# Kernel optimization log

Hardware: AMD Instinct MI355X
Metric: run time of the kernel (lower is better)

The kernel has to match this reference:

```python
import jax, jax.numpy as jnp
import numpy as np

B, L, D = 2, 2048, 1024
H = 16
DEPTH = D // H  # 64
MAX_REL = 2048


def _make_relative_embedding():
    length = max(MAX_REL, DEPTH)
    r = np.arange(length)
    mat = np.clip(r[None, :] - r[:, None], -MAX_REL, MAX_REL) + MAX_REL
    return jnp.asarray(mat[:MAX_REL, :DEPTH], dtype=jnp.float32)


def setup_inputs() -> dict:
    key = jax.random.key(0)
    ks = jax.random.split(key, 8)
    query = jax.random.normal(ks[0], (B, L, D), dtype=jnp.float32)
    k_in = jax.random.normal(ks[1], (B, L, D), dtype=jnp.float32)
    v_in = jax.random.normal(ks[2], (B, L, D), dtype=jnp.float32)
    mask = jnp.tril(jnp.ones((L, L), dtype=bool))  # causal mask (memory_len, memory_len)
    Wq = jax.random.normal(ks[3], (D, D), dtype=jnp.float32) * 0.02
    bq = jnp.zeros((D,), dtype=jnp.float32)
    Wo = jax.random.normal(ks[4], (D, D), dtype=jnp.float32) * 0.02
    bo = jnp.zeros((D,), dtype=jnp.float32)
    rel_emb = _make_relative_embedding()  # [MAX_REL, DEPTH]
    return {"query": query, "key": k_in, "value": v_in, "mask": mask,
            "Wq": Wq, "bq": bq, "Wo": Wo, "bo": bo, "rel_emb": rel_emb}


def _split_heads(x):
    b, l, _ = x.shape
    return x.reshape(b, l, H, DEPTH).transpose(0, 2, 1, 3)  # [b,h,l,depth]


def _skew(rel_logits, length_k):
    # rel_logits: [b,h,Lq,Lq] (square by construction)
    b, h, lq, _ = rel_logits.shape
    x = jnp.pad(rel_logits, ((0, 0), (0, 0), (0, 0), (1, 0)))  # pad left on last dim
    x = x.reshape(b, h, lq + 1, lq)[:, :, 1:, :]
    if length_k > lq:
        x = jnp.pad(x, ((0, 0), (0, 0), (0, 0), (0, length_k - lq)))
    elif length_k < lq:
        x = x[:, :, :, :length_k]
    return x


def reference(query, key, value, mask, Wq, bq, Wo, bo, rel_emb):
    # NOTE: the source module (faithfully) uses query_projection for Q, K and V.
    q = _split_heads(query @ Wq.T + bq)   # [b,h,Lq,d]
    k = _split_heads(key @ Wq.T + bq)     # [b,h,Lk,d]
    v = _split_heads(value @ Wq.T + bq)   # [b,h,Lk,d]
    length_q, length_k = q.shape[2], k.shape[2]

    logits = jnp.einsum('bhqd,bhkd->bhqk', q, k)
    # relative embedding slice: last `length_q` rows (length_q <= MAX_REL)
    start = max(0, MAX_REL - length_q)
    key_rel = rel_emb[start:, :]                            # [Lq, d]
    rel_logits = jnp.einsum('bhld,md->bhlm', q, key_rel)    # [b,h,Lq,Lq]
    rel_logits = _skew(rel_logits, length_k)
    logits = (logits + rel_logits) / jnp.sqrt(jnp.float32(DEPTH))
    logits = jnp.where(mask, logits, jnp.float32(-1e9))
    weights = jax.nn.softmax(logits, axis=-1)               # dropout = identity (eval)
    out = jnp.einsum('bhqk,bhkd->bhqd', weights, v)
    out = out.transpose(0, 2, 1, 3).reshape(out.shape[0], -1, D)
    return out @ Wo.T + bo, weights
```

## Files before the change

### kernel.cpp

```cpp
#include <hip/hip_runtime.h>
#include <cstdint>

#define BB 2
#define LL 2048
#define DD 1024
#define HH 16
#define DH 64
#define BH 32
#define MPROJ 12288
#define MOUT 4096

typedef __attribute__((ext_vector_type(8))) short bhalf8;
typedef __attribute__((ext_vector_type(4))) float f32x4;

__device__ __forceinline__ unsigned short f2bf(float f) {
  union { float f; unsigned u; } c; c.f = f;
  unsigned u = c.u;
  u = (u + 0x7fffu + ((u >> 16) & 1u)) >> 16;
  return (unsigned short)u;
}

constexpr size_t OFF_XBF    = 0;
constexpr size_t OFF_WQBF   = OFF_XBF    + (size_t)MPROJ*DD*2;
constexpr size_t OFF_WOBF   = OFF_WQBF   + (size_t)DD*DD*2;
constexpr size_t OFF_QBF    = OFF_WOBF   + (size_t)DD*DD*2;
constexpr size_t OFF_KBF    = OFF_QBF    + (size_t)BH*LL*DH*2;
constexpr size_t OFF_VTBF   = OFF_KBF    + (size_t)BH*LL*DH*2;
constexpr size_t OFF_ATTNBF = OFF_VTBF   + (size_t)BH*LL*DH*2;
constexpr size_t OFF_WAS    = OFF_ATTNBF + (size_t)MOUT*DD*2;
constexpr size_t OFF_BAS    = OFF_WAS    + (size_t)2*HH*DD*4;
constexpr size_t OFF_AARR   = OFF_BAS    + 256;
constexpr size_t OFF_SARR   = OFF_AARR   + (size_t)BH*LL*4;
constexpr size_t OFF_MARR   = OFF_SARR   + (size_t)BH*LL*4;
constexpr size_t OFF_ZARR   = OFF_MARR   + (size_t)BH*LL*4;
constexpr size_t WS_NEED    = OFF_ZARR   + (size_t)BH*LL*4;

__global__ __launch_bounds__(256) void cast_f32_bf16(
    const float* __restrict__ src, unsigned short* __restrict__ dst, int n4) {
  int i = blockIdx.x * 256 + threadIdx.x;
  if (i < n4) {
    float4 v = ((const float4*)src)[i];
    ushort4 o;
    o.x = f2bf(v.x); o.y = f2bf(v.y); o.z = f2bf(v.z); o.w = f2bf(v.w);
    ((ushort4*)dst)[i] = o;
  }
}

__global__ __launch_bounds__(256) void prep_rel(
    const float* __restrict__ Wq, const float* __restrict__ bq,
    const float* __restrict__ rel, float* __restrict__ wAS, float* __restrict__ bAS) {
  int idx = blockIdx.x * 256 + threadIdx.x;
  if (idx >= 2 * HH * DD) return;
  int kind = idx >> 14;
  int h = (idx >> 10) & 15;
  int c = idx & 1023;
  double s = 0.0;
  for (int d = 0; d < DH; ++d) {
    double coef = kind ? 1.0 : (double)rel[d];
    s += coef * (double)Wq[(size_t)(h * DH + d) * DD + c];
  }
  wAS[idx] = (float)s;
  if (c == 0) {
    double b = 0.0;
    for (int d = 0; d < DH; ++d) {
      double coef = kind ? 1.0 : (double)rel[d];
      b += coef * (double)bq[h * DH + d];
    }
    bAS[kind * HH + h] = (float)b;
  }
}

__global__ __launch_bounds__(256) void rel_AS(
    const float* __restrict__ query, const float* __restrict__ wAS,
    const float* __restrict__ bAS, float* __restrict__ A_arr, float* __restrict__ S_arr) {
  int r = blockIdx.x * 8 + (threadIdx.x >> 5);
  int j = threadIdx.x & 31;
  const float* qrow = query + (size_t)r * DD;
  const float* w = wAS + (size_t)j * DD;
  double s = 0.0;
  for (int k = 0; k < DD; k += 4) {
    float4 qv = *(const float4*)(qrow + k);
    float4 wv = *(const float4*)(w + k);
    s += (double)qv.x * wv.x + (double)qv.y * wv.y +
         (double)qv.z * wv.z + (double)qv.w * wv.w;
  }
  s += (double)bAS[j];
  int b = r >> 11, l = r & 2047;
  int h = j & 15;
  size_t idx = (size_t)(b * HH + h) * LL + l;
  if (j >> 4) S_arr[idx] = (float)s; else A_arr[idx] = (float)s;
}

template <int EPI>
__global__ __launch_bounds__(256) void gemm_bt(
    const unsigned short* __restrict__ A, const unsigned short* __restrict__ Bm,
    const float* __restrict__ bias,
    unsigned short* __restrict__ q_bf, unsigned short* __restrict__ k_bf,
    unsigned short* __restrict__ vt_bf, float* __restrict__ outp) {
  __shared__ unsigned short lA[2][128 * 32];
  __shared__ unsigned short lB[2][128 * 32];
  const int bi = blockIdx.x, bj = blockIdx.y;
  const int t = threadIdx.x;
  const int w = t >> 6, lane = t & 63;
  const int lr = lane & 15, kg = lane >> 4;
  const int wr = w >> 1, wc = w & 1;

  const int srow = t >> 1, scol = (t & 1) * 16;
  const unsigned short* gA = A + (size_t)(bi * 128 + srow) * DD + scol;
  const unsigned short* gB = Bm + (size_t)(bj * 128 + srow) * DD + scol;
  const int soff = srow * 32 + scol;

  const f32x4 Z4 = {0.f, 0.f, 0.f, 0.f};
  f32x4 acc[4][4];
#pragma unroll
  for (int m = 0; m < 4; ++m)
#pragma unroll
    for (int n = 0; n < 4; ++n) acc[m][n] = Z4;

  {
    uint4 ra0 = *(const uint4*)(gA);
    uint4 ra1 = *(const uint4*)(gA + 8);
    uint4 rb0 = *(const uint4*)(gB);
    uint4 rb1 = *(const uint4*)(gB + 8);
    *(uint4*)&lA[0][soff] = ra0; *(uint4*)&lA[0][soff + 8] = ra1;
    *(uint4*)&lB[0][soff] = rb0; *(uint4*)&lB[0][soff + 8] = rb1;
  }
  __syncthreads();

  int cur = 0;
  for (int kt = 0; kt < 32; ++kt) {
    uint4 ra0, ra1, rb0, rb1;
    const bool more = (kt + 1 < 32);
    if (more) {
      const int k0 = (kt + 1) * 32;
      ra0 = *(const uint4*)(gA + k0);
      ra1 = *(const uint4*)(gA + k0 + 8);
      rb0 = *(const uint4*)(gB + k0);
      rb1 = *(const uint4*)(gB + k0 + 8);
    }
    bhalf8 af[4], bf[4];
#pragma unroll
    for (int m = 0; m < 4; ++m)
      af[m] = *(const bhalf8*)&lA[cur][(wr * 64 + m * 16 + lr) * 32 + kg * 8];
#pragma unroll
    for (int n = 0; n < 4; ++n)
      bf[n] = *(const bhalf8*)&lB[cur][(wc * 64 + n * 16 + lr) * 32 + kg * 8];
#pragma unroll
    for (int m = 0; m < 4; ++m)
#pragma unroll
      for (int n = 0; n < 4; ++n)
        acc[m][n] = __builtin_amdgcn_mfma_f32_16x16x32_bf16(af[m], bf[n], acc[m][n], 0, 0, 0);
    if (more) {
      *(uint4*)&lA[cur ^ 1][soff] = ra0; *(uint4*)&lA[cur ^ 1][soff + 8] = ra1;
      *(uint4*)&lB[cur ^ 1][soff] = rb0; *(uint4*)&lB[cur ^ 1][soff + 8] = rb1;
    }
    __syncthreads();
    cur ^= 1;
  }

#pragma unroll
  for (int n = 0; n < 4; ++n) {
    const int gcol = bj * 128 + wc * 64 + n * 16 + lr;
    const float bv = bias[gcol];
#pragma unroll
    for (int m = 0; m < 4; ++m) {
#pragma unroll
      for (int r = 0; r < 4; ++r) {
        const int grow = bi * 128 + wr * 64 + m * 16 + kg * 4 + r;
        float v = acc[m][n][r] + bv;
        if (EPI == 0) {
          const int src = grow >> 12;
          const int rl = grow & 4095;
          const int b = rl >> 11, l2 = rl & 2047;
          const int h = gcol >> 6, d = gcol & 63;
          const int bh = b * HH + h;
          unsigned short bfv = f2bf(v);
          if (src == 0)      q_bf[((size_t)bh * LL + l2) * DH + d] = bfv;
          else if (src == 1) k_bf[((size_t)bh * LL + l2) * DH + d] = bfv;
          else               vt_bf[((size_t)bh * DH + d) * LL + l2] = bfv;
        } else {
          outp[(size_t)grow * DD + gcol] = v;
        }
      }
    }
  }
}


__global__ __launch_bounds__(256) void attn_a(
    const unsigned short* __restrict__ q_bf, const unsigned short* __restrict__ k_bf,
    const float* __restrict__ A_arr, const float* __restrict__ S_arr,
    float* __restrict__ M_arr, float* __restrict__ Zinv_arr) {
  __shared__ unsigned short lK[2][64 * 64];
  const int bid = blockIdx.x;
  const int bh = bid & 31, qt = 31 - (bid >> 5);
  const int t = threadIdx.x, w = t >> 6, lane = t & 63;
  const int lr = lane & 15, kg = lane >> 4;
  const int qrow0 = qt * 64 + w * 16;

  const unsigned short* qbase = q_bf + ((size_t)bh * LL + qrow0 + lr) * DH + kg * 8;
  bhalf8 aq0 = *(const bhalf8*)qbase;
  bhalf8 aq1 = *(const bhalf8*)(qbase + 32);

  float Av[4], Sv[4], Mr[4], ps[4];
  int myrow[4];
#pragma unroll
  for (int r = 0; r < 4; ++r) {
    myrow[r] = qrow0 + kg * 4 + r;
    Av[r] = A_arr[(size_t)bh * LL + myrow[r]];
    Sv[r] = S_arr[(size_t)bh * LL + myrow[r]];
    Mr[r] = -INFINITY; ps[r] = 0.f;
  }

  const int srow = t >> 2, scol = (t & 3) * 16;
  const int se0 = srow * 64 + ((((t & 3) * 2 + 0) ^ (srow & 7)) * 8);
  const int se1 = srow * 64 + ((((t & 3) * 2 + 1) ^ (srow & 7)) * 8);
  const unsigned short* kbase = k_bf + (size_t)bh * LL * DH;
  const f32x4 Z4 = {0.f, 0.f, 0.f, 0.f};

  {
    const unsigned short* src = kbase + (size_t)srow * DH + scol;
    uint4 v0 = *(const uint4*)src;
    uint4 v1 = *(const uint4*)(src + 8);
    *(uint4*)&lK[0][se0] = v0;
    *(uint4*)&lK[0][se1] = v1;
  }

  int cur = 0;
  for (int kt = 0; kt <= qt; ++kt) {
    __syncthreads();
    uint4 n0, n1;
    const bool more = (kt < qt);
    if (more) {
      const unsigned short* src = kbase + (size_t)((kt + 1) * 64 + srow) * DH + scol;
      n0 = *(const uint4*)src;
      n1 = *(const uint4*)(src + 8);
    }
    f32x4 acc[4];
#pragma unroll
    for (int n = 0; n < 4; ++n) {
      acc[n] = Z4;
      const int rowb = n * 16 + lr;
      bhalf8 b0 = *(const bhalf8*)&lK[cur][rowb * 64 + ((kg ^ (rowb & 7)) * 8)];
      bhalf8 b1 = *(const bhalf8*)&lK[cur][rowb * 64 + (((4 + kg) ^ (rowb & 7)) * 8)];
      acc[n] = __builtin_amdgcn_mfma_f32_16x16x32_bf16(aq0, b0, acc[n], 0, 0, 0);
      acc[n] = __builtin_amdgcn_mfma_f32_16x16x32_bf16(aq1, b1, acc[n], 0, 0, 0);
    }
    float lg[4][4];
#pragma unroll
    for (int n = 0; n < 4; ++n) {
      const int gcol = kt * 64 + n * 16 + lr;
#pragma unroll
      for (int r = 0; r < 4; ++r) {
        float rel = Av[r] - (float)(2047 - myrow[r] + gcol) * Sv[r];
        float l = (acc[n][r] + rel) * 0.125f;
        lg[n][r] = (gcol <= myrow[r]) ? l : -1e30f;
      }
    }
#pragma unroll
    for (int r = 0; r < 4; ++r) {
      float tmax = fmaxf(fmaxf(lg[0][r], lg[1][r]), fmaxf(lg[2][r], lg[3][r]));
      tmax = fmaxf(tmax, __shfl_xor(tmax, 1));
      tmax = fmaxf(tmax, __shfl_xor(tmax, 2));
      tmax = fmaxf(tmax, __shfl_xor(tmax, 4));
      tmax = fmaxf(tmax, __shfl_xor(tmax, 8));
      float Mn = fmaxf(Mr[r], tmax);
      float s = ps[r] * __expf(Mr[r] - Mn);
      s += __expf(lg[0][r] - Mn) + __expf(lg[1][r] - Mn) +
           __expf(lg[2][r] - Mn) + __expf(lg[3][r] - Mn);
      ps[r] = s; Mr[r] = Mn;
    }
    if (more) {
      *(uint4*)&lK[cur ^ 1][se0] = n0;
      *(uint4*)&lK[cur ^ 1][se1] = n1;
    }
    cur ^= 1;
  }
#pragma unroll
  for (int r = 0; r < 4; ++r) {
    float s = ps[r];
    s += __shfl_xor(s, 1); s += __shfl_xor(s, 2);
    s += __shfl_xor(s, 4); s += __shfl_xor(s, 8);
    if (lr == 0) {
      M_arr[(size_t)bh * LL + myrow[r]] = Mr[r];
      Zinv_arr[(size_t)bh * LL + myrow[r]] = 1.0f / s;
    }
  }
}

__global__ __launch_bounds__(256) void attn_b(
    const unsigned short* __restrict__ q_bf, const unsigned short* __restrict__ k_bf,
    const unsigned short* __restrict__ vt_bf,
    const float* __restrict__ A_arr, const float* __restrict__ S_arr,
    const float* __restrict__ M_arr, const float* __restrict__ Zinv_arr,
    float* __restrict__ w_out, unsigned short* __restrict__ attn_bf) {
  __shared__ unsigned short lK[2][64 * 64];
  __shared__ unsigned short lW[64][72];
  const int bid = blockIdx.x;
  const int bh = bid & 31, qt = 31 - (bid >> 5);
  const int t = threadIdx.x, w = t >> 6, lane = t & 63;
  const int lr = lane & 15, kg = lane >> 4;
  const int qrow0 = qt * 64 + w * 16;

  const unsigned short* qbase = q_bf + ((size_t)bh * LL + qrow0 + lr) * DH + kg * 8;
  bhalf8 aq0 = *(const bhalf8*)qbase;
  bhalf8 aq1 = *(const bhalf8*)(qbase + 32);

  float Av[4], Sv[4], Mv[4], Zv[4];
  int myrow[4];
#pragma unroll
  for (int r = 0; r < 4; ++r) {
    myrow[r] = qrow0 + kg * 4 + r;
    Av[r] = A_arr[(size_t)bh * LL + myrow[r]];
    Sv[r] = S_arr[(size_t)bh * LL + myrow[r]];
    Mv[r] = M_arr[(size_t)bh * LL + myrow[r]];
    Zv[r] = Zinv_arr[(size_t)bh * LL + myrow[r]];
  }

  const f32x4 Z4 = {0.f, 0.f, 0.f, 0.f};
  f32x4 oacc[4];
#pragma unroll
  for (int n = 0; n < 4; ++n) oacc[n] = Z4;

  const int srow = t >> 2, scol = (t & 3) * 16;
  const int se0 = srow * 64 + ((((t & 3) * 2 + 0) ^ (srow & 7)) * 8);
  const int se1 = srow * 64 + ((((t & 3) * 2 + 1) ^ (srow & 7)) * 8);
  const unsigned short* kbase = k_bf + (size_t)bh * LL * DH;
  const unsigned short* vtb = vt_bf + (size_t)bh * DH * LL;

  for (int kt = qt + 1; kt < 32; ++kt) {
    float* dst = w_out + ((size_t)bh * LL + qt * 64 + srow) * LL + kt * 64 + scol;
    float4 z = make_float4(0.f, 0.f, 0.f, 0.f);
    *(float4*)(dst) = z; *(float4*)(dst + 4) = z;
    *(float4*)(dst + 8) = z; *(float4*)(dst + 12) = z;
  }

  {
    const unsigned short* src = kbase + (size_t)srow * DH + scol;
    uint4 v0 = *(const uint4*)src;
    uint4 v1 = *(const uint4*)(src + 8);
    *(uint4*)&lK[0][se0] = v0;
    *(uint4*)&lK[0][se1] = v1;
  }

  int cur = 0;
  for (int kt = 0; kt <= qt; ++kt) {
    __syncthreads();
    uint4 n0, n1;
    const bool more = (kt < qt);
    if (more) {
      const unsigned short* src = kbase + (size_t)((kt + 1) * 64 + srow) * DH + scol;
      n0 = *(const uint4*)src;
      n1 = *(const uint4*)(src + 8);
    }
    f32x4 acc[4];
#pragma unroll
    for (int n = 0; n < 4; ++n) {
      acc[n] = Z4;
      const int rowb = n * 16 + lr;
      bhalf8 b0 = *(const bhalf8*)&lK[cur][rowb * 64 + ((kg ^ (rowb & 7)) * 8)];
      bhalf8 b1 = *(const bhalf8*)&lK[cur][rowb * 64 + (((4 + kg) ^ (rowb & 7)) * 8)];
      acc[n] = __builtin_amdgcn_mfma_f32_16x16x32_bf16(aq0, b0, acc[n], 0, 0, 0);
      acc[n] = __builtin_amdgcn_mfma_f32_16x16x32_bf16(aq1, b1, acc[n], 0, 0, 0);
    }
#pragma unroll
    for (int n = 0; n < 4; ++n) {
      const int gcol = kt * 64 + n * 16 + lr;
#pragma unroll
      for (int r = 0; r < 4; ++r) {
        float rel = Av[r] - (float)(2047 - myrow[r] + gcol) * Sv[r];
        float l = (acc[n][r] + rel) * 0.125f;
        float wgt = (gcol <= myrow[r]) ? __expf(l - Mv[r]) * Zv[r] : 0.f;
        lW[w * 16 + kg * 4 + r][n * 16 + lr] = f2bf(wgt);
        w_out[((size_t)bh * LL + myrow[r]) * LL + gcol] = wgt;
      }
    }
    bhalf8 aw0 = *(const bhalf8*)&lW[w * 16 + lr][kg * 8];
    bhalf8 aw1 = *(const bhalf8*)&lW[w * 16 + lr][32 + kg * 8];
#pragma unroll
    for (int n = 0; n < 4; ++n) {
      const unsigned short* vp = vtb + (size_t)(n * 16 + lr) * LL + kt * 64 + kg * 8;
      bhalf8 bv0 = *(const bhalf8*)vp;
      bhalf8 bv1 = *(const bhalf8*)(vp + 32);
      oacc[n] = __builtin_amdgcn_mfma_f32_16x16x32_bf16(aw0, bv0, oacc[n], 0, 0, 0);
      oacc[n] = __builtin_amdgcn_mfma_f32_16x16x32_bf16(aw1, bv1, oacc[n], 0, 0, 0);
    }
    if (more) {
      *(uint4*)&lK[cur ^ 1][se0] = n0;
      *(uint4*)&lK[cur ^ 1][se1] = n1;
    }
    cur ^= 1;
  }
  const int b = bh >> 4, h = bh & 15;
#pragma unroll
  for (int n = 0; n < 4; ++n)
#pragma unroll
    for (int r = 0; r < 4; ++r)
      attn_bf[(size_t)(b * LL + myrow[r]) * DD + h * DH + n * 16 + lr] = f2bf(oacc[n][r]);
}

extern "C" void kernel_launch(void* const* d_in, const int* in_sizes, int n_in,
                              void* d_out, int out_size, void* d_ws, size_t ws_size,
                              hipStream_t stream) {
  const float* query = (const float*)d_in[0];
  const float* key   = (const float*)d_in[1];
  const float* value = (const float*)d_in[2];
  const float* Wq = (const float*)d_in[4];
  const float* bq = (const float*)d_in[5];
  const float* Wo = (const float*)d_in[6];
  const float* bo = (const float*)d_in[7];
  const float* rel = (const float*)d_in[8];

  if (ws_size < WS_NEED) return;

  char* ws = (char*)d_ws;
  unsigned short* Xbf    = (unsigned short*)(ws + OFF_XBF);
  unsigned short* Wqbf   = (unsigned short*)(ws + OFF_WQBF);
  unsigned short* Wobf   = (unsigned short*)(ws + OFF_WOBF);
  unsigned short* q_bf   = (unsigned short*)(ws + OFF_QBF);
  unsigned short* k_bf   = (unsigned short*)(ws + OFF_KBF);
  unsigned short* vt_bf  = (unsigned short*)(ws + OFF_VTBF);
  unsigned short* attnbf = (unsigned short*)(ws + OFF_ATTNBF);
  float* wAS   = (float*)(ws + OFF_WAS);
  float* bAS   = (float*)(ws + OFF_BAS);
  float* A_arr = (float*)(ws + OFF_AARR);
  float* S_arr = (float*)(ws + OFF_SARR);
  float* M_arr = (float*)(ws + OFF_MARR);
  float* Z_arr = (float*)(ws + OFF_ZARR);

  float* out0 = (float*)d_out;
  float* w_out = out0 + (size_t)MOUT * DD;

  cast_f32_bf16<<<4096, 256, 0, stream>>>(query, Xbf, 1048576);
  cast_f32_bf16<<<4096, 256, 0, stream>>>(key,   Xbf + (size_t)MOUT * DD, 1048576);
  cast_f32_bf16<<<4096, 256, 0, stream>>>(value, Xbf + (size_t)2 * MOUT * DD, 1048576);
  cast_f32_bf16<<<1024, 256, 0, stream>>>(Wq, Wqbf, 262144);
  cast_f32_bf16<<<1024, 256, 0, stream>>>(Wo, Wobf, 262144);

  prep_rel<<<128, 256, 0, stream>>>(Wq, bq, rel, wAS, bAS);
  rel_AS<<<512, 256, 0, stream>>>(query, wAS, bAS, A_arr, S_arr);

  gemm_bt<0><<<dim3(96, 8), 256, 0, stream>>>(Xbf, Wqbf, bq, q_bf, k_bf, vt_bf, nullptr);

  attn_a<<<1024, 256, 0, stream>>>(q_bf, k_bf, A_arr, S_arr, M_arr, Z_arr);
  attn_b<<<1024, 256, 0, stream>>>(q_bf, k_bf, vt_bf, A_arr, S_arr, M_arr, Z_arr,
                                   w_out, attnbf);

  gemm_bt<1><<<dim3(32, 8), 256, 0, stream>>>(attnbf, Wobf, bo, nullptr, nullptr, nullptr, out0);
}
```

Baseline: 1.029 ms.

## Use direct global-to-LDS async loads in GEMM and attention kernels, defer softmax reductions

Replaces the register-staged double-buffer loads in the projection GEMM and both attention passes with global_load_lds 16-byte async copies. The XOR-swizzled layout for K is kept by permuting the global source address instead of the LDS destination. This frees VGPRs and removes the LDS store instructions. In the first attention pass, the per-tile cross-lane max shuffles are dropped: each lane keeps its own running max and sum, and these are merged once at the end with a log-sum-exp butterfly. That cuts shuffle and exp work per tile. The risk is synchronisation correctness, since there is no explicit vmcnt wait before the barrier, so the async LDS writes may not be complete when the data is read.

```diff
diff --git a/kernel.cpp b/kernel.cpp
--- a/kernel.cpp
+++ b/kernel.cpp
@@ -18,6 +18,12 @@
   unsigned u = c.u;
   u = (u + 0x7fffu + ((u >> 16) & 1u)) >> 16;
   return (unsigned short)u;
+}
+
+__device__ __forceinline__ void async_copy16(void* lds, const void* g) {
+  __builtin_amdgcn_global_load_lds(
+      (const __attribute__((address_space(1))) unsigned int*)g,
+      (__attribute__((address_space(3))) unsigned int*)lds, 16, 0, 0);
 }
 
 constexpr size_t OFF_XBF    = 0;
@@ -105,10 +111,11 @@
   const int lr = lane & 15, kg = lane >> 4;
   const int wr = w >> 1, wc = w & 1;
 
-  const int srow = t >> 1, scol = (t & 1) * 16;
-  const unsigned short* gA = A + (size_t)(bi * 128 + srow) * DD + scol;
-  const unsigned short* gB = Bm + (size_t)(bj * 128 + srow) * DD + scol;
-  const int soff = srow * 32 + scol;
+  const unsigned short* gAb = A + (size_t)(bi * 128) * DD;
+  const unsigned short* gBb = Bm + (size_t)(bj * 128) * DD;
+  const int c0 = w * 128 + lane;
+  const int row0 = c0 >> 2, q0 = (c0 & 3) * 8;
+  const int row1 = (c0 + 64) >> 2, q1 = ((c0 + 64) & 3) * 8;
 
   const f32x4 Z4 = {0.f, 0.f, 0.f, 0.f};
   f32x4 acc[4][4];
@@ -118,25 +125,21 @@
     for (int n = 0; n < 4; ++n) acc[m][n] = Z4;
 
   {
-    uint4 ra0 = *(const uint4*)(gA);
-    uint4 ra1 = *(const uint4*)(gA + 8);
-    uint4 rb0 = *(const uint4*)(gB);
-    uint4 rb1 = *(const uint4*)(gB + 8);
-    *(uint4*)&lA[0][soff] = ra0; *(uint4*)&lA[0][soff + 8] = ra1;
-    *(uint4*)&lB[0][soff] = rb0; *(uint4*)&lB[0][soff + 8] = rb1;
-  }
-  __syncthreads();
+    async_copy16(&lA[0][(w * 128) * 8],      gAb + (size_t)row0 * DD + q0);
+    async_copy16(&lA[0][(w * 128 + 64) * 8], gAb + (size_t)row1 * DD + q1);
+    async_copy16(&lB[0][(w * 128) * 8],      gBb + (size_t)row0 * DD + q0);
+    async_copy16(&lB[0][(w * 128 + 64) * 8], gBb + (size_t)row1 * DD + q1);
+  }
 
   int cur = 0;
   for (int kt = 0; kt < 32; ++kt) {
-    uint4 ra0, ra1, rb0, rb1;
-    const bool more = (kt + 1 < 32);
-    if (more) {
+    __syncthreads();
+    if (kt + 1 < 32) {
       const int k0 = (kt + 1) * 32;
-      ra0 = *(const uint4*)(gA + k0);
-      ra1 = *(const uint4*)(gA + k0 + 8);
-      rb0 = *(const uint4*)(gB + k0);
-      rb1 = *(const uint4*)(gB + k0 + 8);
+      async_copy16(&lA[cur ^ 1][(w * 128) * 8],      gAb + (size_t)row0 * DD + k0 + q0);
+      async_copy16(&lA[cur ^ 1][(w * 128 + 64) * 8], gAb + (size_t)row1 * DD + k0 + q1);
+      async_copy16(&lB[cur ^ 1][(w * 128) * 8],      gBb + (size_t)row0 * DD + k0 + q0);
+      async_copy16(&lB[cur ^ 1][(w * 128 + 64) * 8], gBb + (size_t)row1 * DD + k0 + q1);
     }
     bhalf8 af[4], bf[4];
 #pragma unroll
@@ -150,11 +153,6 @@
 #pragma unroll
       for (int n = 0; n < 4; ++n)
         acc[m][n] = __builtin_amdgcn_mfma_f32_16x16x32_bf16(af[m], bf[n], acc[m][n], 0, 0, 0);
-    if (more) {
-      *(uint4*)&lA[cur ^ 1][soff] = ra0; *(uint4*)&lA[cur ^ 1][soff + 8] = ra1;
-      *(uint4*)&lB[cur ^ 1][soff] = rb0; *(uint4*)&lB[cur ^ 1][soff + 8] = rb1;
-    }
-    __syncthreads();
     cur ^= 1;
   }
 
@@ -202,39 +200,34 @@
   bhalf8 aq0 = *(const bhalf8*)qbase;
   bhalf8 aq1 = *(const bhalf8*)(qbase + 32);
 
-  float Av[4], Sv[4], Mr[4], ps[4];
+  float Av[4], Sv[4], Ml[4], sl[4];
   int myrow[4];
 #pragma unroll
   for (int r = 0; r < 4; ++r) {
     myrow[r] = qrow0 + kg * 4 + r;
     Av[r] = A_arr[(size_t)bh * LL + myrow[r]];
     Sv[r] = S_arr[(size_t)bh * LL + myrow[r]];
-    Mr[r] = -INFINITY; ps[r] = 0.f;
-  }
-
-  const int srow = t >> 2, scol = (t & 3) * 16;
-  const int se0 = srow * 64 + ((((t & 3) * 2 + 0) ^ (srow & 7)) * 8);
-  const int se1 = srow * 64 + ((((t & 3) * 2 + 1) ^ (srow & 7)) * 8);
+    Ml[r] = -INFINITY; sl[r] = 0.f;
+  }
+
   const unsigned short* kbase = k_bf + (size_t)bh * LL * DH;
+  const int ca = w * 128 + lane;
+  const int rowA = ca >> 3, chA = ((ca & 7) ^ (rowA & 7)) * 8;
+  const int cb = ca + 64;
+  const int rowB = cb >> 3, chB = ((cb & 7) ^ (rowB & 7)) * 8;
   const f32x4 Z4 = {0.f, 0.f, 0.f, 0.f};
 
-  {
-    const unsigned short* src = kbase + (size_t)srow * DH + scol;
-    uint4 v0 = *(const uint4*)src;
-    uint4 v1 = *(const uint4*)(src + 8);
-    *(uint4*)&lK[0][se0] = v0;
-    *(uint4*)&lK[0][se1] = v1;
-  }
+  async_copy16(&lK[0][(w * 128) * 8],      kbase + (size_t)rowA * DH + chA);
+  async_copy16(&lK[0][(w * 128 + 64) * 8], kbase + (size_t)rowB * DH + chB);
 
   int cur = 0;
   for (int kt = 0; kt <= qt; ++kt) {
     __syncthreads();
-    uint4 n0, n1;
-    const bool more = (kt < qt);
-    if (more) {
-      const unsigned short* src = kbase + (size_t)((kt + 1) * 64 + srow) * DH + scol;
-      n0 = *(const uint4*)src;
-      n1 = *(const uint4*)(src + 8);
+    if (kt < qt) {
+      async_copy16(&lK[cur ^ 1][(w * 128) * 8],
+                   kbase + (size_t)((kt + 1) * 64 + rowA) * DH + chA);
+      async_copy16(&lK[cur ^ 1][(w * 128 + 64) * 8],
+                   kbase + (size_t)((kt + 1) * 64 + rowB) * DH + chB);
     }
     f32x4 acc[4];
 #pragma unroll
@@ -246,43 +239,38 @@
       acc[n] = __builtin_amdgcn_mfma_f32_16x16x32_bf16(aq0, b0, acc[n], 0, 0, 0);
       acc[n] = __builtin_amdgcn_mfma_f32_16x16x32_bf16(aq1, b1, acc[n], 0, 0, 0);
     }
-    float lg[4][4];
-#pragma unroll
-    for (int n = 0; n < 4; ++n) {
-      const int gcol = kt * 64 + n * 16 + lr;
-#pragma unroll
-      for (int r = 0; r < 4; ++r) {
+#pragma unroll
+    for (int r = 0; r < 4; ++r) {
+      float lg[4];
+#pragma unroll
+      for (int n = 0; n < 4; ++n) {
+        const int gcol = kt * 64 + n * 16 + lr;
         float rel = Av[r] - (float)(2047 - myrow[r] + gcol) * Sv[r];
         float l = (acc[n][r] + rel) * 0.125f;
-        lg[n][r] = (gcol <= myrow[r]) ? l : -1e30f;
+        lg[n] = (gcol <= myrow[r]) ? l : -1e30f;
       }
-    }
-#pragma unroll
-    for (int r = 0; r < 4; ++r) {
-      float tmax = fmaxf(fmaxf(lg[0][r], lg[1][r]), fmaxf(lg[2][r], lg[3][r]));
-      tmax = fmaxf(tmax, __shfl_xor(tmax, 1));
-      tmax = fmaxf(tmax, __shfl_xor(tmax, 2));
-      tmax = fmaxf(tmax, __shfl_xor(tmax, 4));
-      tmax = fmaxf(tmax, __shfl_xor(tmax, 8));
-      float Mn = fmaxf(Mr[r], tmax);
-      float s = ps[r] * __expf(Mr[r] - Mn);
-      s += __expf(lg[0][r] - Mn) + __expf(lg[1][r] - Mn) +
-           __expf(lg[2][r] - Mn) + __expf(lg[3][r] - Mn);
-      ps[r] = s; Mr[r] = Mn;
-    }
-    if (more) {
-      *(uint4*)&lK[cur ^ 1][se0] = n0;
-      *(uint4*)&lK[cur ^ 1][se1] = n1;
+      float m4 = fmaxf(fmaxf(lg[0], lg[1]), fmaxf(lg[2], lg[3]));
+      float Mn = fmaxf(Ml[r], m4);
+      sl[r] = sl[r] * __expf(Ml[r] - Mn) +
+              __expf(lg[0] - Mn) + __expf(lg[1] - Mn) +
+              __expf(lg[2] - Mn) + __expf(lg[3] - Mn);
+      Ml[r] = Mn;
     }
     cur ^= 1;
   }
 #pragma unroll
   for (int r = 0; r < 4; ++r) {
-    float s = ps[r];
-    s += __shfl_xor(s, 1); s += __shfl_xor(s, 2);
-    s += __shfl_xor(s, 4); s += __shfl_xor(s, 8);
+    float M = Ml[r], s = sl[r];
+#pragma unroll
+    for (int d = 1; d < 16; d <<= 1) {
+      float Mo = __shfl_xor(M, d);
+      float so = __shfl_xor(s, d);
+      float Mn = fmaxf(M, Mo);
+      s = s * __expf(M - Mn) + so * __expf(Mo - Mn);
+      M = Mn;
+    }
     if (lr == 0) {
-      M_arr[(size_t)bh * LL + myrow[r]] = Mr[r];
+      M_arr[(size_t)bh * LL + myrow[r]] = M;
       Zinv_arr[(size_t)bh * LL + myrow[r]] = 1.0f / s;
     }
   }
@@ -322,36 +310,32 @@
 #pragma unroll
   for (int n = 0; n < 4; ++n) oacc[n] = Z4;
 
-  const int srow = t >> 2, scol = (t & 3) * 16;
-  const int se0 = srow * 64 + ((((t & 3) * 2 + 0) ^ (srow & 7)) * 8);
-  const int se1 = srow * 64 + ((((t & 3) * 2 + 1) ^ (srow & 7)) * 8);
   const unsigned short* kbase = k_bf + (size_t)bh * LL * DH;
   const unsigned short* vtb = vt_bf + (size_t)bh * DH * LL;
-
+  const int ca = w * 128 + lane;
+  const int rowA = ca >> 3, chA = ((ca & 7) ^ (rowA & 7)) * 8;
+  const int cb = ca + 64;
+  const int rowB = cb >> 3, chB = ((cb & 7) ^ (rowB & 7)) * 8;
+
+  const int drow = t >> 2, dcol = (t & 3) * 16;
   for (int kt = qt + 1; kt < 32; ++kt) {
-    float* dst = w_out + ((size_t)bh * LL + qt * 64 + srow) * LL + kt * 64 + scol;
+    float* dst = w_out + ((size_t)bh * LL + qt * 64 + drow) * LL + kt * 64 + dcol;
     float4 z = make_float4(0.f, 0.f, 0.f, 0.f);
     *(float4*)(dst) = z; *(float4*)(dst + 4) = z;
     *(float4*)(dst + 8) = z; *(float4*)(dst + 12) = z;
   }
 
-  {
-    const unsigned short* src = kbase + (size_t)srow * DH + scol;
-    uint4 v0 = *(const uint4*)src;
-    uint4 v1 = *(const uint4*)(src + 8);
-    *(uint4*)&lK[0][se0] = v0;
-    *(uint4*)&lK[0][se1] = v1;
-  }
+  async_copy16(&lK[0][(w * 128) * 8],      kbase + (size_t)rowA * DH + chA);
+  async_copy16(&lK[0][(w * 128 + 64) * 8], kbase + (size_t)rowB * DH + chB);
 
   int cur = 0;
   for (int kt = 0; kt <= qt; ++kt) {
     __syncthreads();
-    uint4 n0, n1;
-    const bool more = (kt < qt);
-    if (more) {
-      const unsigned short* src = kbase + (size_t)((kt + 1) * 64 + srow) * DH + scol;
-      n0 = *(const uint4*)src;
-      n1 = *(const uint4*)(src + 8);
+    if (kt < qt) {
+      async_copy16(&lK[cur ^ 1][(w * 128) * 8],
+                   kbase + (size_t)((kt + 1) * 64 + rowA) * DH + chA);
+      async_copy16(&lK[cur ^ 1][(w * 128 + 64) * 8],
+                   kbase + (size_t)((kt + 1) * 64 + rowB) * DH + chB);
     }
     f32x4 acc[4];
 #pragma unroll
@@ -384,10 +368,6 @@
       bhalf8 bv1 = *(const bhalf8*)(vp + 32);
       oacc[n] = __builtin_amdgcn_mfma_f32_16x16x32_bf16(aw0, bv0, oacc[n], 0, 0, 0);
       oacc[n] = __builtin_amdgcn_mfma_f32_16x16x32_bf16(aw1, bv1, oacc[n], 0, 0, 0);
-    }
-    if (more) {
-      *(uint4*)&lK[cur ^ 1][se0] = n0;
-      *(uint4*)&lK[cur ^ 1][se1] = n1;
     }
     cur ^= 1;
   }
```

Measured after the change: 1.018 ms. About the same (-1.1%).
